# Kernel optimization log

Hardware: AMD Instinct MI355X
Metric: run time of the kernel (lower is better)

## Reference

```python
import jax, jax.numpy as jnp
import numpy as np

B, H, N, M, S, R, BANKS = 64, 1024, 65536, 64, 3, 4, 4
EPS_COS = 1e-8   # cosine-similarity epsilon
EPS_NORM = 1e-5  # final weight normalization epsilon (from original code)


def setup_inputs() -> dict:
    key = jax.random.key(0)
    ks = jax.random.split(key, 12)
    w = lambda k, s: jax.random.normal(k, s, jnp.float32) * 0.02
    return dict(
        h_t=jax.random.normal(ks[0], (B, H), jnp.float32),
        ww=jax.nn.softmax(jax.random.uniform(ks[1], (B, N), jnp.float32), axis=-1),
        wr=jax.nn.softmax(jax.random.uniform(ks[2], (R, B, N), jnp.float32), axis=-1),
        memory=jax.random.uniform(ks[3], (BANKS, N, M), jnp.float32) * 0.1,
        key_w=w(ks[4], (H, M)), key_b=jnp.zeros((M,), jnp.float32),
        beta_w=w(ks[5], (H, 1)), beta_b=jnp.zeros((1,), jnp.float32),
        gate_w=w(ks[6], (H, 1)), gate_b=jnp.zeros((1,), jnp.float32),
        shift_w=w(ks[7], (H, S)), shift_b=jnp.zeros((S,), jnp.float32),
        gamma_w=w(ks[8], (H, 1)), gamma_b=jnp.zeros((1,), jnp.float32),
        erase_w=w(ks[9], (H, M)), erase_b=jnp.zeros((M,), jnp.float32),
        add_w=w(ks[10], (H, M)), add_b=jnp.zeros((M,), jnp.float32),
        bank_no=0,
    )


def _weight_update(h, w_tm1, m, key_w, key_b, beta_w, beta_b, gate_w, gate_b,
                   shift_w, shift_b, gamma_w, gamma_b):
    # h: [B,H], w_tm1: [B,N], m: [N,M]
    k = jnp.clip(h @ key_w + key_b, 0.0, 1.0)            # [B,M] key
    beta = jax.nn.relu(h @ beta_w + beta_b)              # [B,1] sharpness
    g = jnp.clip(h @ gate_w + gate_b, 0.0, 1.0)          # [B,1] interpolation gate
    s = jax.nn.softmax(h @ shift_w + shift_b, axis=-1)   # [B,S] shift kernel
    gamma = 1.0 + jax.nn.relu(h @ gamma_w + gamma_b)     # [B,1] sharpening power
    # content addressing: cosine similarity of key against each memory row
    kn = k / (jnp.linalg.norm(k, axis=1, keepdims=True) + EPS_COS)
    mn = m / (jnp.linalg.norm(m, axis=1, keepdims=True) + EPS_COS)
    sim = kn @ mn.T                                      # [B,N]
    w_c = jax.nn.softmax(sim * beta, axis=-1)            # [B,N]
    w_g = g * w_c + (1.0 - g) * w_tm1                    # gated interpolation
    # per-sample 1D shift (cross-correlation, zero-padded to keep length N)
    pad_l = S // 2
    w_pad = jnp.pad(w_g, ((0, 0), (pad_l, S - 1 - pad_l)))
    shifted = jnp.stack([w_pad[:, j:j + N] for j in range(S)], axis=1)  # [B,S,N]
    w_tilde = jnp.einsum('bs,bsn->bn', s, shifted)
    # power sharpening; normalization by GLOBAL sum (quirk of the original code)
    w_pow = w_tilde ** gamma
    return w_pow / (jnp.sum(w_pow) + EPS_NORM)


def reference(h_t, ww, wr, memory, key_w, key_b, beta_w, beta_b, gate_w, gate_b,
              shift_w, shift_b, gamma_w, gamma_b, erase_w, erase_b, add_w, add_b,
              bank_no):
    m0 = memory[bank_no]                                  # [N,M]
    wu = lambda w_prev, m: _weight_update(
        h_t, w_prev, m, key_w, key_b, beta_w, beta_b, gate_w, gate_b,
        shift_w, shift_b, gamma_w, gamma_b)
    # write head
    ww_new = wu(ww, m0)                                   # [B,N]
    e = jnp.clip(h_t @ erase_w + erase_b, 0.0, 1.0)       # [B,M] erase vec
    a = jnp.clip(jax.nn.relu(h_t @ add_w + add_b), 0.0, 1.0)  # [B,M] add vec
    # batched outer-product erase/add (replaces the python torch.ger loop)
    mem_erase = jnp.einsum('bn,bm->nm', ww_new, e)
    mem_add = jnp.einsum('bn,bm->nm', ww_new, a)
    m1 = m0 * (1.0 - mem_erase) + mem_add                 # [N,M]
    # read heads (vmapped over num_reads)
    wr_new = jax.vmap(lambda wp: wu(wp, m1))(wr)          # [R,B,N]
    r = jnp.einsum('rbn,nm->rbm', wr_new, m1)             # [R,B,M]
    r_t = jnp.transpose(r, (1, 0, 2)).reshape(B, R * M)   # cat along dim 1
    return r_t
```

## Files before the change

### kernel.cpp

```cpp
#include <hip/hip_runtime.h>

#define NN 65536
#define BB 64
#define HH 1024
#define MM 64
#define RR 4

__device__ __forceinline__ float waveReduceSum(float v) {
#pragma unroll
  for (int off = 32; off > 0; off >>= 1) v += __shfl_xor(v, off, 64);
  return v;
}

__device__ __forceinline__ float fastPow(float wt, float p) {
  return __expf(p * __logf(wt));
}

__global__ __launch_bounds__(256) void prep1_kernel(
    const float* __restrict__ h_t,
    const float* __restrict__ key_w, const float* __restrict__ erase_w,
    const float* __restrict__ add_w,
    float* __restrict__ prep_part,
    float* __restrict__ RS0p, float* __restrict__ RS1p, float* __restrict__ GSp)
{
  const int b = blockIdx.y;
  const int mat = blockIdx.x >> 2, chunk = blockIdx.x & 3;
  const int t = threadIdx.x;
  if (mat == 0 && chunk == 0) { RS0p[b * 256 + t] = 0.f; RS1p[b * 256 + t] = 0.f; }
  if (mat == 0 && chunk == 1 && b < 20) GSp[b * 256 + t] = 0.f;

  const float* Wm = (mat == 0) ? key_w : ((mat == 1) ? erase_w : add_w);
  const int c = t & 63, q = t >> 6;
  const int h0 = chunk * 256 + q * 64;
  float d = 0.f;
#pragma unroll 8
  for (int i = 0; i < 64; i++)
    d += h_t[b * HH + h0 + i] * Wm[(h0 + i) * 64 + c];
  __shared__ float red[64][5];
  red[c][q] = d;
  __syncthreads();
  if (t < 64)
    prep_part[((b * 3 + mat) * 4 + chunk) * 64 + t] =
        red[t][0] + red[t][1] + red[t][2] + red[t][3];
}

__global__ __launch_bounds__(256) void prep2_kernel(
    const float* __restrict__ h_t, const float* __restrict__ prep_part,
    const float* __restrict__ key_b,
    const float* __restrict__ beta_w, const float* __restrict__ beta_b,
    const float* __restrict__ gate_w, const float* __restrict__ gate_b,
    const float* __restrict__ shift_w, const float* __restrict__ shift_b,
    const float* __restrict__ gamma_w, const float* __restrict__ gamma_b,
    const float* __restrict__ erase_b, const float* __restrict__ add_b,
    float* __restrict__ kn, float* __restrict__ e_v, float* __restrict__ a_v,
    float* __restrict__ g, float* __restrict__ gamma_,
    float* __restrict__ s, float* __restrict__ betaGlob)
{
  const int b = blockIdx.x;
  const int t = threadIdx.x;
  __shared__ float k_sh[64];
  if (t < 192) {
    const int mat = t >> 6, c = t & 63;
    const float* pp = prep_part + ((b * 3 + mat) * 4) * 64 + c;
    const float v = pp[0] + pp[64] + pp[128] + pp[192];
    if (mat == 0) k_sh[c] = fminf(fmaxf(v + key_b[c], 0.f), 1.f);
    else if (mat == 1) e_v[b * 64 + c] = fminf(fmaxf(v + erase_b[c], 0.f), 1.f);
    else a_v[b * 64 + c] = fminf(fmaxf(v + add_b[c], 0.f), 1.f);
  } else {
    const int lane = t - 192;
    float o0 = 0.f, o1 = 0.f, o2 = 0.f, o3 = 0.f, o4 = 0.f, o5 = 0.f;
#pragma unroll 4
    for (int k = 0; k < 16; k++) {
      const int hh = lane + k * 64;
      const float hv = h_t[b * HH + hh];
      o0 += hv * beta_w[hh];
      o1 += hv * gate_w[hh];
      o2 += hv * gamma_w[hh];
      o3 += hv * shift_w[hh * 3 + 0];
      o4 += hv * shift_w[hh * 3 + 1];
      o5 += hv * shift_w[hh * 3 + 2];
    }
    o0 = waveReduceSum(o0); o1 = waveReduceSum(o1); o2 = waveReduceSum(o2);
    o3 = waveReduceSum(o3); o4 = waveReduceSum(o4); o5 = waveReduceSum(o5);
    if (lane == 0) {
      betaGlob[b] = fmaxf(o0 + beta_b[0], 0.f);
      g[b]        = fminf(fmaxf(o1 + gate_b[0], 0.f), 1.f);
      gamma_[b]   = 1.0f + fmaxf(o2 + gamma_b[0], 0.f);
      const float l0 = o3 + shift_b[0], l1 = o4 + shift_b[1], l2 = o5 + shift_b[2];
      const float mx = fmaxf(l0, fmaxf(l1, l2));
      const float e0 = __expf(l0 - mx), e1 = __expf(l1 - mx), e2 = __expf(l2 - mx);
      const float inv = 1.f / (e0 + e1 + e2);
      s[b * 3 + 0] = e0 * inv; s[b * 3 + 1] = e1 * inv; s[b * 3 + 2] = e2 * inv;
    }
  }
  __syncthreads();
  if (t < 64) {
    float ss = 0.f;
    for (int j = 0; j < 64; j++) ss += k_sh[j] * k_sh[j];
    kn[b * 64 + t] = k_sh[t] / (sqrtf(ss) + 1e-8f);
  }
}

__global__ __launch_bounds__(256, 4) void content_kernel(
    const float* __restrict__ mem, const int* __restrict__ bank,
    const float* __restrict__ kn, const float* __restrict__ beta,
    float* __restrict__ E, float* __restrict__ RSp)
{
  const float* Mrow = mem + (bank ? ((size_t)(*bank) * (size_t)NN * MM) : (size_t)0);
  const int t = threadIdx.x;
  const int lane = t & 63;
  const int n = blockIdx.x * 64 + lane;
  const int bq = t >> 6;

  float4 row[16];
  const float4* rp = (const float4*)(Mrow + (size_t)n * MM);
#pragma unroll
  for (int q = 0; q < 16; q++) row[q] = rp[q];
  float s0 = 0.f, s1 = 0.f, s2 = 0.f, s3 = 0.f;
#pragma unroll
  for (int q = 0; q < 16; q++) {
    s0 += row[q].x * row[q].x; s1 += row[q].y * row[q].y;
    s2 += row[q].z * row[q].z; s3 += row[q].w * row[q].w;
  }
  const float rinv = 1.0f / (sqrtf((s0 + s1) + (s2 + s3)) + 1e-8f);

#pragma unroll 2
  for (int i = 0; i < 16; i++) {
    const int rb = __builtin_amdgcn_readfirstlane(bq * 16 + i);
    const float4* kp = (const float4*)(kn + rb * 64);
    float d0 = 0.f, d1 = 0.f, d2 = 0.f, d3 = 0.f;
#pragma unroll
    for (int q = 0; q < 16; q++) {
      const float4 kq = kp[q];
      d0 += kq.x * row[q].x; d1 += kq.y * row[q].y;
      d2 += kq.z * row[q].z; d3 += kq.w * row[q].w;
    }
    const float e = __expf(beta[rb] * ((d0 + d1) + (d2 + d3)) * rinv);
    E[(size_t)rb * NN + n] = e;
    const float r = waveReduceSum(e);
    if (lane == 0)
      atomicAdd(&RSp[rb * 256 + (blockIdx.x & 15) * 16], r);
  }
}

template <int NR>
__global__ __launch_bounds__(256) void wpow_all_kernel(
    const float* __restrict__ E, const float* __restrict__ wprev,
    const float* __restrict__ RSp, const float* __restrict__ g,
    const float* __restrict__ gamma_, const float* __restrict__ s,
    float* __restrict__ Wout, float* __restrict__ GSp, int slot0)
{
  const int b = blockIdx.y;
  const float gb = g[b], gmb = gamma_[b];
  const float s0 = s[b * 3], s1 = s[b * 3 + 1], s2 = s[b * 3 + 2];
  float rs = 0.f;
#pragma unroll
  for (int j = 0; j < 16; j++) rs += RSp[b * 256 + j * 16];
  const float grinv = gb / rs;
  const float omg = 1.f - gb;

  const int t = threadIdx.x, lane = t & 63, w = t >> 6;
  const int n4 = blockIdx.x * 1024 + 4 * t;

  const float* Eb = E + (size_t)b * NN;
  const float4 ev = *((const float4*)(Eb + n4));
  const float gex = grinv * ev.x, gey = grinv * ev.y;
  const float gez = grinv * ev.z, gew = grinv * ev.w;
  float geL = 0.f, geR = 0.f;
  if (lane == 0 && n4 > 0) geL = grinv * Eb[n4 - 1];
  if (lane == 63 && n4 + 4 < NN) geR = grinv * Eb[n4 + 4];

  float gs_local[NR];
#pragma unroll
  for (int j = 0; j < NR; j++) gs_local[j] = 0.f;

#pragma unroll
  for (int j = 0; j < NR; j++) {
    const float* wb = wprev + ((size_t)j * BB + b) * NN;
    const float4 wv = *((const float4*)(wb + n4));
    float4 wgc;
    wgc.x = gex + omg * wv.x;
    wgc.y = gey + omg * wv.y;
    wgc.z = gez + omg * wv.z;
    wgc.w = gew + omg * wv.w;
    float up = __shfl_up(wgc.w, 1, 64);
    float dn = __shfl_down(wgc.x, 1, 64);
    if (lane == 0)  up = (n4 > 0)       ? (geL + omg * wb[n4 - 1]) : 0.f;
    if (lane == 63) dn = (n4 + 4 < NN)  ? (geR + omg * wb[n4 + 4]) : 0.f;
    float4 wt;
    wt.x = s0 * up    + s1 * wgc.x + s2 * wgc.y;
    wt.y = s0 * wgc.x + s1 * wgc.y + s2 * wgc.z;
    wt.z = s0 * wgc.y + s1 * wgc.z + s2 * wgc.w;
    wt.w = s0 * wgc.z + s1 * wgc.w + s2 * dn;
    float4 wp;
    wp.x = fastPow(wt.x, gmb); wp.y = fastPow(wt.y, gmb);
    wp.z = fastPow(wt.z, gmb); wp.w = fastPow(wt.w, gmb);
    *((float4*)(Wout + ((size_t)j * BB + b) * NN + n4)) = wp;
    gs_local[j] += wp.x + wp.y + wp.z + wp.w;
  }

  __shared__ float wsum[4][NR];
#pragma unroll
  for (int j = 0; j < NR; j++) {
    const float v = waveReduceSum(gs_local[j]);
    if (lane == 0) wsum[w][j] = v;
  }
  __syncthreads();
  if (t < NR)
    atomicAdd(&GSp[(slot0 + t) * 1024 + b * 16],
              wsum[0][t] + wsum[1][t] + wsum[2][t] + wsum[3][t]);
}

__global__ __launch_bounds__(256) void apply_write_kernel(
    const float* __restrict__ W0, const float* __restrict__ GSp,
    const float* __restrict__ e_v, const float* __restrict__ a_v,
    const float* __restrict__ memory, const int* __restrict__ bank,
    float* __restrict__ m1)
{
  __shared__ float cw[64 * 68];
  __shared__ float e_sh[4096];
  __shared__ float a_sh[4096];
  const int t = threadIdx.x;
  const int n0 = blockIdx.x * 64;
  float gs = 0.f;
#pragma unroll
  for (int j = 0; j < 64; j++) gs += GSp[j * 16];
  const float invGS = 1.0f / (gs + 1e-5f);
#pragma unroll
  for (int q = 0; q < 4; q++) {
    ((float4*)e_sh)[t + 256 * q] = ((const float4*)e_v)[t + 256 * q];
    ((float4*)a_sh)[t + 256 * q] = ((const float4*)a_v)[t + 256 * q];
  }
#pragma unroll
  for (int rep = 0; rep < 4; rep++) {
    const int idx = rep * 256 + t;
    const int b = idx >> 4, nc = idx & 15;
    float4 v = *((const float4*)(W0 + (size_t)b * NN + n0 + nc * 4));
    v.x *= invGS; v.y *= invGS; v.z *= invGS; v.w *= invGS;
    *((float4*)&cw[b * 68 + nc * 4]) = v;
  }
  __syncthreads();
  const int nl = t >> 2, mq = t & 3;
  const int n = n0 + nl;
  float er[16], ad[16];
#pragma unroll
  for (int j = 0; j < 16; j++) { er[j] = 0.f; ad[j] = 0.f; }
  for (int b = 0; b < 64; b++) {
    const float c = cw[b * 68 + nl];
#pragma unroll
    for (int j = 0; j < 4; j++) {
      const float4 ev = *((const float4*)&e_sh[b * 64 + mq * 16 + j * 4]);
      const float4 av = *((const float4*)&a_sh[b * 64 + mq * 16 + j * 4]);
      er[j * 4 + 0] += c * ev.x; er[j * 4 + 1] += c * ev.y;
      er[j * 4 + 2] += c * ev.z; er[j * 4 + 3] += c * ev.w;
      ad[j * 4 + 0] += c * av.x; ad[j * 4 + 1] += c * av.y;
      ad[j * 4 + 2] += c * av.z; ad[j * 4 + 3] += c * av.w;
    }
  }
  const float* M0 = memory + (size_t)(*bank) * (size_t)NN * MM;
  const float4* m0p = (const float4*)(M0 + (size_t)n * MM + mq * 16);
  float4* m1p = (float4*)(m1 + (size_t)n * MM + mq * 16);
#pragma unroll
  for (int j = 0; j < 4; j++) {
    const float4 mv = m0p[j];
    float4 o;
    o.x = mv.x * (1.f - er[j * 4 + 0]) + ad[j * 4 + 0];
    o.y = mv.y * (1.f - er[j * 4 + 1]) + ad[j * 4 + 1];
    o.z = mv.z * (1.f - er[j * 4 + 2]) + ad[j * 4 + 2];
    o.w = mv.w * (1.f - er[j * 4 + 3]) + ad[j * 4 + 3];
    m1p[j] = o;
  }
}

__global__ __launch_bounds__(256) void gemm_all_kernel(
    const float* __restrict__ W_all, const float* __restrict__ m1,
    float* __restrict__ part)
{
  const int t = threadIdx.x;
  const int mq = t & 15, bq = t >> 4;
  const int n0 = blockIdx.x * 128;
  const int r0 = blockIdx.y * 2;
  __shared__ float m1_sh[64][68];
  __shared__ float w_sh[64][68];
  float4 acc[2][4];
#pragma unroll
  for (int rr = 0; rr < 2; rr++)
#pragma unroll
    for (int j = 0; j < 4; j++) acc[rr][j] = make_float4(0.f, 0.f, 0.f, 0.f);

  for (int sub = 0; sub < 2; ++sub) {
    const int nb = n0 + sub * 64;
    __syncthreads();
#pragma unroll
    for (int rep = 0; rep < 4; rep++) {
      const int nl2 = rep * 16 + bq;
      *((float4*)&m1_sh[nl2][mq * 4]) =
          ((const float4*)(m1 + (size_t)(nb + nl2) * MM))[mq];
    }
    for (int rr = 0; rr < 2; ++rr) {
      __syncthreads();
#pragma unroll
      for (int rep = 0; rep < 4; rep++) {
        const int idx = rep * 256 + t;
        const int b = idx >> 4, nc = idx & 15;
        *((float4*)&w_sh[b][nc * 4]) =
            *((const float4*)(W_all + ((size_t)(r0 + rr) * BB + b) * NN + nb + nc * 4));
      }
      __syncthreads();
#pragma unroll 2
      for (int c4 = 0; c4 < 16; c4++) {
        const int nn = c4 * 4;
        const float4 mv0 = *((const float4*)&m1_sh[nn + 0][mq * 4]);
        const float4 mv1 = *((const float4*)&m1_sh[nn + 1][mq * 4]);
        const float4 mv2 = *((const float4*)&m1_sh[nn + 2][mq * 4]);
        const float4 mv3 = *((const float4*)&m1_sh[nn + 3][mq * 4]);
#pragma unroll
        for (int j = 0; j < 4; j++) {
          const float4 wj = *((const float4*)&w_sh[bq * 4 + j][nn]);
          float4& a = acc[rr][j];
          a.x += wj.x * mv0.x + wj.y * mv1.x + wj.z * mv2.x + wj.w * mv3.x;
          a.y += wj.x * mv0.y + wj.y * mv1.y + wj.z * mv2.y + wj.w * mv3.y;
          a.z += wj.x * mv0.z + wj.y * mv1.z + wj.z * mv2.z + wj.w * mv3.z;
          a.w += wj.x * mv0.w + wj.y * mv1.w + wj.z * mv2.w + wj.w * mv3.w;
        }
      }
    }
  }
#pragma unroll
  for (int rr = 0; rr < 2; rr++)
#pragma unroll
    for (int j = 0; j < 4; j++)
      *((float4*)&part[((size_t)blockIdx.x * 4 + r0 + rr) * 4096 +
                       (bq * 4 + j) * 64 + mq * 4]) = acc[rr][j];
}

__global__ __launch_bounds__(1024) void reduce_norm_kernel(
    const float* __restrict__ part, const float* __restrict__ GSp,
    float* __restrict__ out)
{
  const int t = threadIdx.x;
  const int ln = t & 63, wv = t >> 6;
  const int off = blockIdx.x * 64 + ln;
  const int r = blockIdx.x >> 6;
  float sm = 0.f;
#pragma unroll 8
  for (int k = wv; k < 512; k += 16) sm += part[(size_t)k * 16384 + off];
  __shared__ float red[16][64];
  red[wv][ln] = sm;
  __syncthreads();
  if (t < 64) {
    float gv = GSp[(1 + r) * 1024 + t * 16];
    gv = waveReduceSum(gv);
    float sum = 0.f;
#pragma unroll
    for (int j = 0; j < 16; j++) sum += red[j][t];
    const int off2 = blockIdx.x * 64 + t;
    const int b = (off2 >> 6) & 63, m = off2 & 63;
    out[b * 256 + r * 64 + m] = sum / (gv + 1e-5f);
  }
}

extern "C" void kernel_launch(void* const* d_in, const int* in_sizes, int n_in,
                              void* d_out, int out_size, void* d_ws, size_t ws_size,
                              hipStream_t stream) {
  (void)in_sizes; (void)n_in; (void)out_size; (void)ws_size;
  const float* h_t    = (const float*)d_in[0];
  const float* ww     = (const float*)d_in[1];
  const float* wr     = (const float*)d_in[2];
  const float* memory = (const float*)d_in[3];
  const float* key_w  = (const float*)d_in[4];
  const float* key_b  = (const float*)d_in[5];
  const float* beta_w = (const float*)d_in[6];
  const float* beta_b = (const float*)d_in[7];
  const float* gate_w = (const float*)d_in[8];
  const float* gate_b = (const float*)d_in[9];
  const float* shift_w = (const float*)d_in[10];
  const float* shift_b = (const float*)d_in[11];
  const float* gamma_w = (const float*)d_in[12];
  const float* gamma_b = (const float*)d_in[13];
  const float* erase_w = (const float*)d_in[14];
  const float* erase_b = (const float*)d_in[15];
  const float* add_w   = (const float*)d_in[16];
  const float* add_b   = (const float*)d_in[17];
  const int*   bank    = (const int*)d_in[18];

  float* ws = (float*)d_ws;
  float* E0    = ws;
  float* part  = ws;
  float* W0    = ws + 4194304;
  float* m1    = ws + 8388608;
  float* E1    = ws + 12582912;
  float* W_all = ws + 16777216;
  float* smallb  = ws + 33554432;
  float* kn       = smallb + 16384;
  float* e_v      = smallb + 20480;
  float* a_v      = smallb + 24576;
  float* betaB    = smallb + 28672;
  float* g        = smallb + 28736;
  float* gam      = smallb + 28800;
  float* s        = smallb + 28864;
  float* RS0p     = smallb + 29120;
  float* RS1p     = smallb + 45504;
  float* GSp      = smallb + 61888;
  float* prep_part = smallb + 67008;

  prep1_kernel<<<dim3(12, 64), 256, 0, stream>>>(h_t, key_w, erase_w, add_w,
                                                 prep_part, RS0p, RS1p, GSp);
  prep2_kernel<<<64, 256, 0, stream>>>(h_t, prep_part, key_b,
                                       beta_w, beta_b, gate_w, gate_b,
                                       shift_w, shift_b, gamma_w, gamma_b,
                                       erase_b, add_b,
                                       kn, e_v, a_v, g, gam, s, betaB);
  content_kernel<<<1024, 256, 0, stream>>>(memory, bank, kn, betaB, E0, RS0p);
  wpow_all_kernel<1><<<dim3(64, 64), 256, 0, stream>>>(E0, ww, RS0p, g, gam, s,
                                                       W0, GSp, 0);
  apply_write_kernel<<<1024, 256, 0, stream>>>(W0, GSp, e_v, a_v, memory, bank, m1);
  content_kernel<<<1024, 256, 0, stream>>>(m1, nullptr, kn, betaB, E1, RS1p);
  wpow_all_kernel<4><<<dim3(64, 64), 256, 0, stream>>>(E1, wr, RS1p, g, gam, s,
                                                       W_all, GSp, 1);
  gemm_all_kernel<<<dim3(512, 2), 256, 0, stream>>>(W_all, m1, part);
  reduce_norm_kernel<<<256, 1024, 0, stream>>>(part, GSp, (float*)d_out);
}
```

Baseline: 171.0 us.

## Fuse read-head weight sharpening into the read GEMM kernel

Read-head weight computation (gated interpolation, 3-tap shift, power sharpening) now happens inside the GEMM kernel, straight into shared memory. The large W_all intermediate in global memory is no longer written and read back, which removes a big round trip of memory traffic and one kernel launch. The per-head normaliser sum is accumulated with atomicAdd into a single GSp slot, and the final kernel reads that slot directly instead of reducing partials. This depends on the slot being zeroed beforehand. It also recomputes the scaled E tile in each of the two y-blocks and adds more barriers to the GEMM loop.

```diff
diff --git a/kernel.cpp b/kernel.cpp
--- a/kernel.cpp
+++ b/kernel.cpp
@@ -272,39 +272,85 @@
   }
 }
 
-__global__ __launch_bounds__(256) void gemm_all_kernel(
-    const float* __restrict__ W_all, const float* __restrict__ m1,
-    float* __restrict__ part)
-{
-  const int t = threadIdx.x;
+__global__ __launch_bounds__(256) void wpow_gemm_kernel(
+    const float* __restrict__ E, const float* __restrict__ wr,
+    const float* __restrict__ RSp, const float* __restrict__ g,
+    const float* __restrict__ gamma_, const float* __restrict__ s,
+    const float* __restrict__ m1, float* __restrict__ part,
+    float* __restrict__ GSp)
+{
+  __shared__ float m1_sh[64][68];
+  __shared__ float ge_sh[64][66];
+  __shared__ float w_sh[64][68];
+  __shared__ float rinv_sh[64], omg_sh[64], gm_sh[64];
+  __shared__ float s0_sh[64], s1_sh[64], s2_sh[64];
+  __shared__ float wsum[4][2];
+
+  const int t = threadIdx.x;
+  const int w = t >> 6, lane = t & 63;
   const int mq = t & 15, bq = t >> 4;
   const int n0 = blockIdx.x * 128;
   const int r0 = blockIdx.y * 2;
-  __shared__ float m1_sh[64][68];
-  __shared__ float w_sh[64][68];
+
+  if (t < 64) {
+    float rs = 0.f;
+#pragma unroll
+    for (int j = 0; j < 16; j++) rs += RSp[t * 256 + j * 16];
+    const float gb = g[t];
+    rinv_sh[t] = gb / rs;
+    omg_sh[t]  = 1.f - gb;
+    gm_sh[t]   = gamma_[t];
+    s0_sh[t] = s[t * 3 + 0];
+    s1_sh[t] = s[t * 3 + 1];
+    s2_sh[t] = s[t * 3 + 2];
+  }
+  __syncthreads();
+
   float4 acc[2][4];
 #pragma unroll
   for (int rr = 0; rr < 2; rr++)
 #pragma unroll
     for (int j = 0; j < 4; j++) acc[rr][j] = make_float4(0.f, 0.f, 0.f, 0.f);
+  float gs_acc[2] = {0.f, 0.f};
 
   for (int sub = 0; sub < 2; ++sub) {
     const int nb = n0 + sub * 64;
-    __syncthreads();
 #pragma unroll
     for (int rep = 0; rep < 4; rep++) {
       const int nl2 = rep * 16 + bq;
       *((float4*)&m1_sh[nl2][mq * 4]) =
           ((const float4*)(m1 + (size_t)(nb + nl2) * MM))[mq];
     }
+#pragma unroll 4
+    for (int i = 0; i < 16; i++) {
+      const int b = w * 16 + i;
+      const float gr = rinv_sh[b];
+      ge_sh[b][1 + lane] = gr * E[(size_t)b * NN + nb + lane];
+      if (lane == 0)
+        ge_sh[b][0] = (nb > 0) ? gr * E[(size_t)b * NN + nb - 1] : 0.f;
+      if (lane == 63)
+        ge_sh[b][65] = (nb + 64 < NN) ? gr * E[(size_t)b * NN + nb + 64] : 0.f;
+    }
+    __syncthreads();
+#pragma unroll
     for (int rr = 0; rr < 2; ++rr) {
-      __syncthreads();
-#pragma unroll
-      for (int rep = 0; rep < 4; rep++) {
-        const int idx = rep * 256 + t;
-        const int b = idx >> 4, nc = idx & 15;
-        *((float4*)&w_sh[b][nc * 4]) =
-            *((const float4*)(W_all + ((size_t)(r0 + rr) * BB + b) * NN + nb + nc * 4));
+      const float* wrr = wr + (size_t)(r0 + rr) * BB * NN;
+#pragma unroll 4
+      for (int i = 0; i < 16; i++) {
+        const int b = w * 16 + i;
+        const float omg = omg_sh[b];
+        const float* wb = wrr + (size_t)b * NN;
+        const float wgc = ge_sh[b][1 + lane] + omg * wb[nb + lane];
+        float wgm = __shfl_up(wgc, 1, 64);
+        float wgp = __shfl_down(wgc, 1, 64);
+        if (lane == 0)
+          wgm = (nb > 0) ? (ge_sh[b][0] + omg * wb[nb - 1]) : 0.f;
+        if (lane == 63)
+          wgp = (nb + 64 < NN) ? (ge_sh[b][65] + omg * wb[nb + 64]) : 0.f;
+        const float wt = s0_sh[b] * wgm + s1_sh[b] * wgc + s2_sh[b] * wgp;
+        const float wp = fastPow(wt, gm_sh[b]);
+        w_sh[b][lane] = wp;
+        gs_acc[rr] += wp;
       }
       __syncthreads();
 #pragma unroll 2
@@ -324,6 +370,7 @@
           a.w += wj.x * mv0.w + wj.y * mv1.w + wj.z * mv2.w + wj.w * mv3.w;
         }
       }
+      __syncthreads();
     }
   }
 #pragma unroll
@@ -332,6 +379,15 @@
     for (int j = 0; j < 4; j++)
       *((float4*)&part[((size_t)blockIdx.x * 4 + r0 + rr) * 4096 +
                        (bq * 4 + j) * 64 + mq * 4]) = acc[rr][j];
+#pragma unroll
+  for (int rr = 0; rr < 2; rr++) {
+    const float v = waveReduceSum(gs_acc[rr]);
+    if (lane == 0) wsum[w][rr] = v;
+  }
+  __syncthreads();
+  if (t < 2)
+    atomicAdd(&GSp[(1 + r0 + t) * 1024],
+              wsum[0][t] + wsum[1][t] + wsum[2][t] + wsum[3][t]);
 }
 
 __global__ __launch_bounds__(1024) void reduce_norm_kernel(
@@ -349,8 +405,7 @@
   red[wv][ln] = sm;
   __syncthreads();
   if (t < 64) {
-    float gv = GSp[(1 + r) * 1024 + t * 16];
-    gv = waveReduceSum(gv);
+    const float gv = GSp[(1 + r) * 1024];
     float sum = 0.f;
 #pragma unroll
     for (int j = 0; j < 16; j++) sum += red[j][t];
@@ -390,8 +445,7 @@
   float* W0    = ws + 4194304;
   float* m1    = ws + 8388608;
   float* E1    = ws + 12582912;
-  float* W_all = ws + 16777216;
-  float* smallb  = ws + 33554432;
+  float* smallb  = ws + 16777216;
   float* kn       = smallb + 16384;
   float* e_v      = smallb + 20480;
   float* a_v      = smallb + 24576;
@@ -416,8 +470,7 @@
                                                        W0, GSp, 0);
   apply_write_kernel<<<1024, 256, 0, stream>>>(W0, GSp, e_v, a_v, memory, bank, m1);
   content_kernel<<<1024, 256, 0, stream>>>(m1, nullptr, kn, betaB, E1, RS1p);
-  wpow_all_kernel<4><<<dim3(64, 64), 256, 0, stream>>>(E1, wr, RS1p, g, gam, s,
-                                                       W_all, GSp, 1);
-  gemm_all_kernel<<<dim3(512, 2), 256, 0, stream>>>(W_all, m1, part);
+  wpow_gemm_kernel<<<dim3(512, 2), 256, 0, stream>>>(E1, wr, RS1p, g, gam, s,
+                                                     m1, part, GSp);
   reduce_norm_kernel<<<256, 1024, 0, stream>>>(part, GSp, (float*)d_out);
 }
```

After: 307.9 us. 1.8x slower.
